# Performance work log

Hardware: AMD Instinct MI355X
Metric: run time of the kernel (lower is better)

Reference implementation:

```python
import jax, jax.numpy as jnp
import numpy as np

GX, GY = 96, 96          # cortical grid (cortial_x_count, cortial_y_count)
RF = 24                  # receptive field height/width (hard-coded in source)
B = 8                    # batch
N = GX * GY
GAMMA_E = 0.9
GAMMA_I = -0.9


def setup_inputs() -> dict:
    key = jax.random.key(0)
    k1, k2, k3, k4, k5 = jax.random.split(key, 5)
    H = (GX - 1) + RF  # 119: unit-stride receptive-field starts
    return {
        "input": jax.random.normal(k1, (B, H, H), dtype=jnp.float32),
        "prev_activity": jax.random.uniform(k2, (B, N), dtype=jnp.float32),
        "afferent_weights": jax.random.normal(k3, (GX, GY, RF, RF), dtype=jnp.float32) * 0.02,
        "W_e": jax.random.normal(k4, (N, N), dtype=jnp.float32) * (1.0 / np.sqrt(N)),
        "W_i": jax.random.normal(k5, (N, N), dtype=jnp.float32) * (1.0 / np.sqrt(N)),
        "rf_x": jnp.arange(GX, dtype=jnp.int32),
        "rf_y": jnp.arange(GY, dtype=jnp.int32),
    }


def reference(input, prev_activity, afferent_weights, W_e, W_i, rf_x, rf_y):
    # --- afferent activation: fused patch gather + per-unit dot ---
    # rows[i, h] = rf_x[i] + h ; cols[j, w] = rf_y[j] + w
    rows = rf_x[:, None] + jnp.arange(RF, dtype=rf_x.dtype)          # [GX, RF]
    cols = rf_y[:, None] + jnp.arange(RF, dtype=rf_y.dtype)          # [GY, RF]
    # patches: [B, GX, GY, RF, RF]
    patches = input[:, rows[:, None, :, None], cols[None, :, None, :]]
    afferent = jnp.einsum('bijhw,ijhw->bij', patches, afferent_weights)
    afferent = afferent.reshape(input.shape[0], -1)                  # [B, N]

    # --- lateral terms (F.linear(x, W) == x @ W.T) ---
    lat_e = prev_activity @ W_e.T
    lat_i = prev_activity @ W_i.T

    total = afferent + GAMMA_E * lat_e + GAMMA_I * lat_i
    # sigmoid_approximation == clamp(min=0) == relu
    return jax.nn.relu(total)
```

## Files before the change

kernel.cpp:

```cpp
#include <hip/hip_runtime.h>

#define GXc 96
#define GYc 96
#define RFc 24
#define Bc 8
#define Nc (GXc * GYc)
#define Hc (GXc - 1 + RFc)
#define IN_IMG (Hc * Hc)
#define RF2 (RFc * RFc)
#define GAMMA 0.9f
#define INV_GAMMA (1.0f / 0.9f)

#define ROWS 2
#define WPB 4
#define RPB (ROWS * WPB)
#define NBLOCKS (Nc / RPB)
#define KW 256
#define NWIN (Nc / KW)

__device__ __forceinline__ float dot4(float4 a, float4 b) {
    return a.x * b.x + a.y * b.y + a.z * b.z + a.w * b.w;
}

#define BODY(J, SR, SW, WCUR, WN2, PREF)                                      \
  {                                                                           \
    float4 q0, q1;                                                            \
    if (PREF) {                                                               \
      const int k2 = ((J) + 2) * KW + koff;                                   \
      q0 = *(const float4*)(prev + sb0 * Nc + k2);                            \
      q1 = *(const float4*)(prev + sb1 * Nc + k2);                            \
      WN2[0] = *(const float4*)(r0e + k2);                                    \
      WN2[1] = *(const float4*)(r1e + k2);                                    \
      WN2[2] = *(const float4*)(r0i + k2);                                    \
      WN2[3] = *(const float4*)(r1i + k2);                                    \
    }                                                                         \
    __builtin_amdgcn_sched_barrier(0);                                        \
    {                                                                         \
      const float4 w0 = make_float4(WCUR[0].x - WCUR[2].x,                    \
                                    WCUR[0].y - WCUR[2].y,                    \
                                    WCUR[0].z - WCUR[2].z,                    \
                                    WCUR[0].w - WCUR[2].w);                   \
      const float4 w1 = make_float4(WCUR[1].x - WCUR[3].x,                    \
                                    WCUR[1].y - WCUR[3].y,                    \
                                    WCUR[1].z - WCUR[3].z,                    \
                                    WCUR[1].w - WCUR[3].w);                   \
      _Pragma("unroll")                                                       \
      for (int b = 0; b < Bc; ++b) {                                          \
        const float4 pb4 = *(const float4*)&pv[SR][b][koff];                  \
        acc[0][b] += dot4(w0, pb4);                                           \
        acc[1][b] += dot4(w1, pb4);                                           \
      }                                                                       \
    }                                                                         \
    __builtin_amdgcn_sched_barrier(0);                                        \
    if (PREF) {                                                               \
      *(float4*)&pv[SW][sb0][koff] = q0;                                      \
      *(float4*)&pv[SW][sb1][koff] = q1;                                      \
    }                                                                         \
    asm volatile("s_waitcnt lgkmcnt(0)" ::: "memory");                        \
    __builtin_amdgcn_s_barrier();                                             \
  }

__global__ __launch_bounds__(256) void cortex_fused_kernel(
    const float* __restrict__ input,
    const float* __restrict__ prev,
    const float* __restrict__ aw,
    const float* __restrict__ We,
    const float* __restrict__ Wi,
    float* __restrict__ out)
{
    __shared__ float pv[3][Bc][KW];

    const int tid  = threadIdx.x;
    const int wave = tid >> 6;
    const int lane = tid & 63;
    const int rowbase = blockIdx.x * RPB + wave * ROWS;
    const int koff = lane << 2;
    const int sb0 = wave * 2;
    const int sb1 = wave * 2 + 1;

    float acc[ROWS][Bc];
#pragma unroll
    for (int r = 0; r < ROWS; ++r)
#pragma unroll
        for (int b = 0; b < Bc; ++b) acc[r][b] = 0.f;

#pragma unroll
    for (int r = 0; r < ROWS; ++r) {
        const int n  = rowbase + r;
        const int gi = n / GYc;
        const int gj = n - gi * GYc;
        const float* awn = aw + (size_t)n * RF2;
        const int base = gi * Hc + gj;
#pragma unroll
        for (int t = 0; t < RF2 / 64; ++t) {
            const int hw = t * 64 + lane;
            const int h  = hw / RFc;
            const int w  = hw - h * RFc;
            const float av = awn[hw] * INV_GAMMA;
            const int off  = base + h * Hc + w;
#pragma unroll
            for (int b = 0; b < Bc; ++b)
                acc[r][b] += input[b * IN_IMG + off] * av;
        }
    }

    const float* r0e = We + (size_t)(rowbase + 0) * Nc;
    const float* r1e = We + (size_t)(rowbase + 1) * Nc;
    const float* r0i = Wi + (size_t)(rowbase + 0) * Nc;
    const float* r1i = Wi + (size_t)(rowbase + 1) * Nc;

    float4 wA[4], wB[4], wCr[4];

    {
        float4 q0 = *(const float4*)(prev + sb0 * Nc + koff);
        float4 q1 = *(const float4*)(prev + sb1 * Nc + koff);
        wA[0] = *(const float4*)(r0e + koff);
        wA[1] = *(const float4*)(r1e + koff);
        wA[2] = *(const float4*)(r0i + koff);
        wA[3] = *(const float4*)(r1i + koff);
        float4 q2 = *(const float4*)(prev + sb0 * Nc + KW + koff);
        float4 q3 = *(const float4*)(prev + sb1 * Nc + KW + koff);
        wB[0] = *(const float4*)(r0e + KW + koff);
        wB[1] = *(const float4*)(r1e + KW + koff);
        wB[2] = *(const float4*)(r0i + KW + koff);
        wB[3] = *(const float4*)(r1i + KW + koff);
        *(float4*)&pv[0][sb0][koff] = q0;
        *(float4*)&pv[0][sb1][koff] = q1;
        *(float4*)&pv[1][sb0][koff] = q2;
        *(float4*)&pv[1][sb1][koff] = q3;
        asm volatile("s_waitcnt lgkmcnt(0)" ::: "memory");
        __builtin_amdgcn_s_barrier();
    }

    for (int t = 0; t < 11; ++t) {
        const int j = 3 * t;
        BODY(j,     0, 2, wA,  wCr, true);
        BODY(j + 1, 1, 0, wB,  wA,  true);
        BODY(j + 2, 2, 1, wCr, wB,  true);
    }
    BODY(33, 0, 2, wA,  wCr, true);
    BODY(34, 1, 0, wB,  wA,  false);
    BODY(35, 2, 1, wCr, wB,  false);

#pragma unroll
    for (int r = 0; r < ROWS; ++r)
#pragma unroll
        for (int b = 0; b < Bc; ++b) {
            float v = acc[r][b];
            v += __shfl_xor(v, 1);
            v += __shfl_xor(v, 2);
            v += __shfl_xor(v, 4);
            v += __shfl_xor(v, 8);
            v += __shfl_xor(v, 16);
            v += __shfl_xor(v, 32);
            if (lane == b * ROWS + r) {
                const float tot = GAMMA * v;
                out[b * Nc + rowbase + r] = tot > 0.f ? tot : 0.f;
            }
        }
}

extern "C" void kernel_launch(void* const* d_in, const int* in_sizes, int n_in,
                              void* d_out, int out_size, void* d_ws, size_t ws_size,
                              hipStream_t stream) {
    const float* input = (const float*)d_in[0];
    const float* prev  = (const float*)d_in[1];
    const float* aw    = (const float*)d_in[2];
    const float* We    = (const float*)d_in[3];
    const float* Wi    = (const float*)d_in[4];
    float* out = (float*)d_out;

    cortex_fused_kernel<<<NBLOCKS, 256, 0, stream>>>(input, prev, aw, We, Wi, out);
}
```

Measured before the change: 156.6 us.

## Use 8-wave blocks with double-buffered LDS and one-chunk-ahead weight prefetch

Doubles the waves per block from 4 to 8, so each wave stages a single batch row of prev_activity into LDS instead of two. The LDS ring drops from three buffers to two. Weight prefetch now runs one 256-wide K chunk ahead instead of two, which frees registers. The aim is more concurrent waves streaming the bandwidth-bound W_e/W_i rows while shrinking per-wave LDS staging work, at the risk of less latency hiding per wave and costlier 512-thread barriers.

```diff
diff --git a/kernel.cpp b/kernel.cpp
--- a/kernel.cpp
+++ b/kernel.cpp
@@ -12,7 +12,7 @@
 #define INV_GAMMA (1.0f / 0.9f)
 
 #define ROWS 2
-#define WPB 4
+#define WPB 8
 #define RPB (ROWS * WPB)
 #define NBLOCKS (Nc / RPB)
 #define KW 256
@@ -22,17 +22,18 @@
     return a.x * b.x + a.y * b.y + a.z * b.z + a.w * b.w;
 }
 
-#define BODY(J, SR, SW, WCUR, WN2, PREF)                                      \
+#define BODY(KBASE, SR, SW, WCUR, WNEXT, QLOAD, QWRITE, PREF_P, PREF_W)       \
   {                                                                           \
-    float4 q0, q1;                                                            \
-    if (PREF) {                                                               \
-      const int k2 = ((J) + 2) * KW + koff;                                   \
-      q0 = *(const float4*)(prev + sb0 * Nc + k2);                            \
-      q1 = *(const float4*)(prev + sb1 * Nc + k2);                            \
-      WN2[0] = *(const float4*)(r0e + k2);                                    \
-      WN2[1] = *(const float4*)(r1e + k2);                                    \
-      WN2[2] = *(const float4*)(r0i + k2);                                    \
-      WN2[3] = *(const float4*)(r1i + k2);                                    \
+    if (PREF_P) {                                                             \
+      const int k2 = (KBASE) + 2 * KW + koff;                                 \
+      QLOAD = *(const float4*)(prev + wave * Nc + k2);                        \
+    }                                                                         \
+    if (PREF_W) {                                                             \
+      const int k1 = (KBASE) + KW + koff;                                     \
+      WNEXT[0] = *(const float4*)(r0e + k1);                                  \
+      WNEXT[1] = *(const float4*)(r1e + k1);                                  \
+      WNEXT[2] = *(const float4*)(r0i + k1);                                  \
+      WNEXT[3] = *(const float4*)(r1i + k1);                                  \
     }                                                                         \
     __builtin_amdgcn_sched_barrier(0);                                        \
     {                                                                         \
@@ -52,15 +53,15 @@
       }                                                                       \
     }                                                                         \
     __builtin_amdgcn_sched_barrier(0);                                        \
-    if (PREF) {                                                               \
-      *(float4*)&pv[SW][sb0][koff] = q0;                                      \
-      *(float4*)&pv[SW][sb1][koff] = q1;                                      \
+    if (PREF_P || PREF_W) {                     \
+      *(float4*)&pv[SW][wave][koff] = QWRITE;                                 \
     }                                                                         \
     asm volatile("s_waitcnt lgkmcnt(0)" ::: "memory");                        \
     __builtin_amdgcn_s_barrier();                                             \
+    __builtin_amdgcn_sched_barrier(0);                                        \
   }
 
-__global__ __launch_bounds__(256) void cortex_fused_kernel(
+__global__ __launch_bounds__(512) void cortex_fused_kernel(
     const float* __restrict__ input,
     const float* __restrict__ prev,
     const float* __restrict__ aw,
@@ -68,15 +69,13 @@
     const float* __restrict__ Wi,
     float* __restrict__ out)
 {
-    __shared__ float pv[3][Bc][KW];
+    __shared__ float pv[2][Bc][KW];
 
     const int tid  = threadIdx.x;
     const int wave = tid >> 6;
     const int lane = tid & 63;
     const int rowbase = blockIdx.x * RPB + wave * ROWS;
     const int koff = lane << 2;
-    const int sb0 = wave * 2;
-    const int sb1 = wave * 2 + 1;
 
     float acc[ROWS][Bc];
 #pragma unroll
@@ -109,38 +108,28 @@
     const float* r0i = Wi + (size_t)(rowbase + 0) * Nc;
     const float* r1i = Wi + (size_t)(rowbase + 1) * Nc;
 
-    float4 wA[4], wB[4], wCr[4];
+    float4 wA[4], wB[4], q0, q1;
 
     {
-        float4 q0 = *(const float4*)(prev + sb0 * Nc + koff);
-        float4 q1 = *(const float4*)(prev + sb1 * Nc + koff);
+        q0 = *(const float4*)(prev + wave * Nc + koff);
+        q1 = *(const float4*)(prev + wave * Nc + KW + koff);
         wA[0] = *(const float4*)(r0e + koff);
         wA[1] = *(const float4*)(r1e + koff);
         wA[2] = *(const float4*)(r0i + koff);
         wA[3] = *(const float4*)(r1i + koff);
-        float4 q2 = *(const float4*)(prev + sb0 * Nc + KW + koff);
-        float4 q3 = *(const float4*)(prev + sb1 * Nc + KW + koff);
-        wB[0] = *(const float4*)(r0e + KW + koff);
-        wB[1] = *(const float4*)(r1e + KW + koff);
-        wB[2] = *(const float4*)(r0i + KW + koff);
-        wB[3] = *(const float4*)(r1i + KW + koff);
-        *(float4*)&pv[0][sb0][koff] = q0;
-        *(float4*)&pv[0][sb1][koff] = q1;
-        *(float4*)&pv[1][sb0][koff] = q2;
-        *(float4*)&pv[1][sb1][koff] = q3;
+        *(float4*)&pv[0][wave][koff] = q0;
         asm volatile("s_waitcnt lgkmcnt(0)" ::: "memory");
         __builtin_amdgcn_s_barrier();
+        __builtin_amdgcn_sched_barrier(0);
     }
 
-    for (int t = 0; t < 11; ++t) {
-        const int j = 3 * t;
-        BODY(j,     0, 2, wA,  wCr, true);
-        BODY(j + 1, 1, 0, wB,  wA,  true);
-        BODY(j + 2, 2, 1, wCr, wB,  true);
+    for (int t = 0; t < 17; ++t) {
+        const int kb0 = (2 * t) * KW;
+        BODY(kb0,      0, 1, wA, wB, q0, q1, true, true);
+        BODY(kb0 + KW, 1, 0, wB, wA, q1, q0, true, true);
     }
-    BODY(33, 0, 2, wA,  wCr, true);
-    BODY(34, 1, 0, wB,  wA,  false);
-    BODY(35, 2, 1, wCr, wB,  false);
+    BODY(34 * KW, 0, 1, wA, wB, q0, q1, false, true);
+    BODY(35 * KW, 1, 0, wB, wA, q1, q0, false, false);
 
 #pragma unroll
     for (int r = 0; r < ROWS; ++r)
@@ -170,5 +159,5 @@
     const float* Wi    = (const float*)d_in[4];
     float* out = (float*)d_out;
 
-    cortex_fused_kernel<<<NBLOCKS, 256, 0, stream>>>(input, prev, aw, We, Wi, out);
+    cortex_fused_kernel<<<NBLOCKS, 512, 0, stream>>>(input, prev, aw, We, Wi, out);
 }
```

New measurement: 191.6 us. +22.4%, slower.
